# Kernel optimization log

Hardware: AMD Instinct MI355X
Metric: run time of the kernel (lower is better)

## Reference

```python
import jax, jax.numpy as jnp
import numpy as np

BS, N, M, D = 4, 8192, 8192, 3

def setup_inputs() -> dict:
    key = jax.random.key(0)
    k1, k2 = jax.random.split(key)
    preds = jax.random.normal(k1, (BS, M, D), dtype=jnp.float32)
    gts = jax.random.normal(k2, (BS, N, D), dtype=jnp.float32)
    mask = jnp.ones((BS, M), dtype=jnp.float32)
    return {"preds": preds, "gts": gts, "mask": mask}

def _pairwise_dist(x, y):
    # x: [bs, N, d] (gts), y: [bs, M, d] (preds)
    # P[b,n,m] = ||x_n||^2 + ||y_m||^2 - 2 x_n . y_m
    rx = jnp.sum(x * x, axis=-1)            # [bs, N] (diag of x @ x^T)
    ry = jnp.sum(y * y, axis=-1)            # [bs, M] (diag of y @ y^T)
    zz = jnp.einsum('bnd,bmd->bnm', x, y)   # [bs, N, M]
    return rx[:, :, None] + ry[:, None, :] - 2.0 * zz

def reference(preds, gts, mask):
    P = _pairwise_dist(gts, preds)          # [bs, N, M]; mask unused (as in source)
    return (jnp.min(P, axis=1),             # [bs, M] min over gts for each pred
            jnp.min(P, axis=2),             # [bs, N] min over preds for each gt
            jnp.argmin(P, axis=1),          # [bs, M]
            jnp.argmin(P, axis=2))          # [bs, N]
```

## Files before the change

### kernel.cpp

```cpp
#include <hip/hip_runtime.h>

#pragma clang fp contract(off)


#define BS     4
#define NPTS   8192
#define CHUNK  2048
#define BLOCK  1024
#define SPLITS 32
#define SLOTS  32
#define QT     8
#define QBLK   (SLOTS * QT)
#define ROWS   (CHUNK / SPLITS)

typedef float f32x2 __attribute__((ext_vector_type(2)));

__global__ __launch_bounds__(BLOCK, 4)
void chamfer_kernel(const float* __restrict__ preds,
                    const float* __restrict__ gts,
                    float* __restrict__ out)
{
#pragma clang fp contract(off)
    const int dir   = blockIdx.z;
    const int b     = blockIdx.y;
    const int t     = threadIdx.x;
    const int slot  = t & (SLOTS - 1);
    const int split = t >> 5;
    const int qb    = blockIdx.x * QBLK;

    const float* qbase = (dir == 0 ? preds : gts) + (size_t)b * NPTS * 3;
    const float* rbase = (dir == 0 ? gts : preds) + (size_t)b * NPTS * 3;
    float* outv = out + (size_t)dir       * BS * NPTS + (size_t)b * NPTS;
    float* outi = out + (size_t)(2 + dir) * BS * NPTS + (size_t)b * NPTS;

    __shared__ alignas(16) float smem[12288];
    float (*sh)[4]        = (float (*)[4])smem;
    float *shv            = smem;
    unsigned short *shi16 = (unsigned short *)(smem + 8192);

    f32x2 qxv[4], qyv[4], qzv[4], rqv[4];
#pragma unroll
    for (int g = 0; g < 4; ++g) {
#pragma unroll
        for (int h = 0; h < 2; ++h) {
            const int j = g * 2 + h;
            const int q = qb + j * SLOTS + slot;
            const float x = qbase[(size_t)q * 3 + 0];
            const float y = qbase[(size_t)q * 3 + 1];
            const float z = qbase[(size_t)q * 3 + 2];
            qxv[g][h] = x; qyv[g][h] = y; qzv[g][h] = z;
            const float a0 = x * x;
            const float a1 = y * y;
            const float a2 = z * z;
            rqv[g][h] = (a0 + a1) + a2;
        }
    }

    float bestv[QT];
    int   besti[QT];
#pragma unroll
    for (int j = 0; j < QT; ++j) { bestv[j] = 3.0e38f; besti[j] = 0; }

    const int nchunks = NPTS / CHUNK;
    for (int c = 0; c < nchunks; ++c) {
        __syncthreads();
#pragma unroll
        for (int u = 0; u < CHUNK / BLOCK; ++u) {
            const int i = u * BLOCK + t;
            const size_t n = (size_t)c * CHUNK + i;
            const float x = rbase[n * 3 + 0];
            const float y = rbase[n * 3 + 1];
            const float z = rbase[n * 3 + 2];
            sh[i][0] = x;
            sh[i][1] = y;
            sh[i][2] = z;
            const float a0 = x * x;
            const float a1 = y * y;
            const float a2 = z * z;
            sh[i][3] = (a0 + a1) + a2;
        }
        __syncthreads();

        const int row0 = split * ROWS;
        const int idxb = c * CHUNK + row0;
#pragma unroll 4
        for (int k = 0; k < ROWS; ++k) {
            const int row = row0 + k;
            const float x  = sh[row][0];
            const float y  = sh[row][1];
            const float z  = sh[row][2];
            const float rr = sh[row][3];
            const int idx = idxb + k;
#pragma unroll
            for (int g = 0; g < 4; ++g) {
                const f32x2 p0 = qxv[g] * x;
                const f32x2 p1 = qyv[g] * y;
                const f32x2 p2 = qzv[g] * z;
                const f32x2 zz = (p0 + p1) + p2;
                const f32x2 ts = rqv[g] + rr;
                const f32x2 w  = zz * 2.0f;
                const f32x2 v  = ts - w;
                if (v[0] < bestv[2 * g + 0]) { bestv[2 * g + 0] = v[0]; besti[2 * g + 0] = idx; }
                if (v[1] < bestv[2 * g + 1]) { bestv[2 * g + 1] = v[1]; besti[2 * g + 1] = idx; }
            }
        }
    }

    __syncthreads();
#pragma unroll
    for (int j = 0; j < QT; ++j) {
        shv  [split * QBLK + j * SLOTS + slot] = bestv[j];
        shi16[split * QBLK + j * SLOTS + slot] = (unsigned short)besti[j];
    }
    __syncthreads();

    const int qloc = t >> 2;
    const int sl   = t & 3;
    float bv = 3.0e38f;
    int   bi = 0;
#pragma unroll
    for (int k = 0; k < SPLITS / 4; ++k) {
        const int s = sl + k * 4;
        const float v2 = shv[s * QBLK + qloc];
        const int   i2 = shi16[s * QBLK + qloc];
        if (v2 < bv || (v2 == bv && i2 < bi)) { bv = v2; bi = i2; }
    }
#pragma unroll
    for (int o = 1; o < 4; o <<= 1) {
        const float ov = __shfl_xor(bv, o);
        const int   oi = __shfl_xor(bi, o);
        if (ov < bv || (ov == bv && oi < bi)) { bv = ov; bi = oi; }
    }
    if (sl == 0) {
        outv[qb + qloc] = bv;
        outi[qb + qloc] = (float)bi;
    }
}

extern "C" void kernel_launch(void* const* d_in, const int* in_sizes, int n_in,
                              void* d_out, int out_size, void* d_ws, size_t ws_size,
                              hipStream_t stream)
{
    const float* preds = (const float*)d_in[0];
    const float* gts   = (const float*)d_in[1];
    float* out = (float*)d_out;

    dim3 grid(NPTS / QBLK, BS, 2);
    dim3 block(BLOCK);
    chamfer_kernel<<<grid, block, 0, stream>>>(preds, gts, out);
}
```

Before: 116.9 us.

## Split reference set into halves with workspace partials and a finalize kernel

The nearest-neighbour search now splits the reference points into two halves. It launches four times as many smaller blocks (512 threads, 128 queries each), each writing its partial min/argmin to a workspace. A small finalize kernel then merges the two halves with a lowest-index tie-break. The goal is more blocks and waves per CU, so the latency of the compare-and-select loop is better hidden. The shared tile is also packed as float4 with padding to cut LDS bank conflicts. The cost is an extra launch and a workspace round trip, and the old single-kernel path is kept as a fallback when the workspace is too small.

```diff
diff --git a/kernel.cpp b/kernel.cpp
--- a/kernel.cpp
+++ b/kernel.cpp
@@ -5,38 +5,40 @@
 
 #define BS     4
 #define NPTS   8192
-#define CHUNK  2048
-#define BLOCK  1024
+#define BLOCK  512
+#define SLOTS  16
 #define SPLITS 32
-#define SLOTS  32
 #define QT     8
 #define QBLK   (SLOTS * QT)
+#define HALF   4096
+#define CHUNK  1024
 #define ROWS   (CHUNK / SPLITS)
 
 typedef float f32x2 __attribute__((ext_vector_type(2)));
+typedef float f32x4 __attribute__((ext_vector_type(4)));
 
 __global__ __launch_bounds__(BLOCK, 4)
-void chamfer_kernel(const float* __restrict__ preds,
-                    const float* __restrict__ gts,
-                    float* __restrict__ out)
+void chamfer_part(const float* __restrict__ preds,
+                  const float* __restrict__ gts,
+                  float* __restrict__ wsv,
+                  unsigned* __restrict__ wsi)
 {
 #pragma clang fp contract(off)
-    const int dir   = blockIdx.z;
-    const int b     = blockIdx.y;
-    const int t     = threadIdx.x;
+    const int dir  = blockIdx.z & 1;
+    const int half = blockIdx.z >> 1;
+    const int b    = blockIdx.y;
+    const int qb   = blockIdx.x * QBLK;
+    const int t    = threadIdx.x;
     const int slot  = t & (SLOTS - 1);
-    const int split = t >> 5;
-    const int qb    = blockIdx.x * QBLK;
+    const int split = t >> 4;
 
     const float* qbase = (dir == 0 ? preds : gts) + (size_t)b * NPTS * 3;
     const float* rbase = (dir == 0 ? gts : preds) + (size_t)b * NPTS * 3;
-    float* outv = out + (size_t)dir       * BS * NPTS + (size_t)b * NPTS;
-    float* outi = out + (size_t)(2 + dir) * BS * NPTS + (size_t)b * NPTS;
-
-    __shared__ alignas(16) float smem[12288];
-    float (*sh)[4]        = (float (*)[4])smem;
-    float *shv            = smem;
-    unsigned short *shi16 = (unsigned short *)(smem + 8192);
+
+    __shared__ alignas(16) float smem[6144];
+    f32x4* tile4          = (f32x4*)smem;
+    float* shv            = smem;
+    unsigned short* shi16 = (unsigned short*)(smem + 4096);
 
     f32x2 qxv[4], qyv[4], qzv[4], rqv[4];
 #pragma unroll
@@ -61,35 +63,34 @@
 #pragma unroll
     for (int j = 0; j < QT; ++j) { bestv[j] = 3.0e38f; besti[j] = 0; }
 
-    const int nchunks = NPTS / CHUNK;
-    for (int c = 0; c < nchunks; ++c) {
+    for (int c = 0; c < HALF / CHUNK; ++c) {
+        const int n0 = half * HALF + c * CHUNK;
         __syncthreads();
 #pragma unroll
         for (int u = 0; u < CHUNK / BLOCK; ++u) {
             const int i = u * BLOCK + t;
-            const size_t n = (size_t)c * CHUNK + i;
+            const size_t n = (size_t)n0 + i;
             const float x = rbase[n * 3 + 0];
             const float y = rbase[n * 3 + 1];
             const float z = rbase[n * 3 + 2];
-            sh[i][0] = x;
-            sh[i][1] = y;
-            sh[i][2] = z;
             const float a0 = x * x;
             const float a1 = y * y;
             const float a2 = z * z;
-            sh[i][3] = (a0 + a1) + a2;
-        }
-        __syncthreads();
-
-        const int row0 = split * ROWS;
-        const int idxb = c * CHUNK + row0;
+            const float rr = (a0 + a1) + a2;
+            const int sp = i + (i >> 5);
+            tile4[sp] = (f32x4){x, y, z, rr};
+        }
+        __syncthreads();
+
+        const int sbase = split * (ROWS + 1);
+        const int idxb  = n0 + split * ROWS;
 #pragma unroll 4
         for (int k = 0; k < ROWS; ++k) {
-            const int row = row0 + k;
-            const float x  = sh[row][0];
-            const float y  = sh[row][1];
-            const float z  = sh[row][2];
-            const float rr = sh[row][3];
+            const f32x4 cand = tile4[sbase + k];
+            const float x  = cand[0];
+            const float y  = cand[1];
+            const float z  = cand[2];
+            const float rr = cand[3];
             const int idx = idxb + k;
 #pragma unroll
             for (int g = 0; g < 4; ++g) {
@@ -132,9 +133,138 @@
         if (ov < bv || (ov == bv && oi < bi)) { bv = ov; bi = oi; }
     }
     if (sl == 0) {
-        outv[qb + qloc] = bv;
-        outi[qb + qloc] = (float)bi;
-    }
+        const size_t g = ((size_t)(dir * BS + b) * NPTS + qb + qloc);
+        wsv[g * 2 + half] = bv;
+        wsi[g * 2 + half] = (unsigned)bi;
+    }
+}
+
+__global__ __launch_bounds__(256)
+void chamfer_fin(const float* __restrict__ wsv,
+                 const unsigned* __restrict__ wsi,
+                 float* __restrict__ out)
+{
+    const int g = blockIdx.x * 256 + threadIdx.x;
+    const float v0 = wsv[2 * g + 0];
+    const float v1 = wsv[2 * g + 1];
+    const unsigned i0 = wsi[2 * g + 0];
+    const unsigned i1 = wsi[2 * g + 1];
+    const bool take1 = (v1 < v0) || (v1 == v0 && i1 < i0);
+    out[g]         = take1 ? v1 : v0;
+    out[65536 + g] = (float)(take1 ? i1 : i0);
+}
+
+#define FCHUNK  2048
+#define FBLOCK  1024
+#define FSPLITS 32
+#define FSLOTS  32
+#define FQBLK   (FSLOTS * QT)
+#define FROWS   (FCHUNK / FSPLITS)
+
+__global__ __launch_bounds__(FBLOCK, 4)
+void chamfer_single(const float* __restrict__ preds,
+                    const float* __restrict__ gts,
+                    float* __restrict__ out)
+{
+#pragma clang fp contract(off)
+    const int dir   = blockIdx.z;
+    const int b     = blockIdx.y;
+    const int t     = threadIdx.x;
+    const int slot  = t & (FSLOTS - 1);
+    const int split = t >> 5;
+    const int qb    = blockIdx.x * FQBLK;
+
+    const float* qbase = (dir == 0 ? preds : gts) + (size_t)b * NPTS * 3;
+    const float* rbase = (dir == 0 ? gts : preds) + (size_t)b * NPTS * 3;
+    float* outv = out + (size_t)dir       * BS * NPTS + (size_t)b * NPTS;
+    float* outi = out + (size_t)(2 + dir) * BS * NPTS + (size_t)b * NPTS;
+
+    __shared__ alignas(16) float smem[12288];
+    float (*sh)[4]        = (float (*)[4])smem;
+    float *shv            = smem;
+    unsigned short *shi16 = (unsigned short *)(smem + 8192);
+
+    f32x2 qxv[4], qyv[4], qzv[4], rqv[4];
+#pragma unroll
+    for (int g = 0; g < 4; ++g) {
+#pragma unroll
+        for (int h = 0; h < 2; ++h) {
+            const int j = g * 2 + h;
+            const int q = qb + j * FSLOTS + slot;
+            const float x = qbase[(size_t)q * 3 + 0];
+            const float y = qbase[(size_t)q * 3 + 1];
+            const float z = qbase[(size_t)q * 3 + 2];
+            qxv[g][h] = x; qyv[g][h] = y; qzv[g][h] = z;
+            const float a0 = x * x, a1 = y * y, a2 = z * z;
+            rqv[g][h] = (a0 + a1) + a2;
+        }
+    }
+
+    float bestv[QT]; int besti[QT];
+#pragma unroll
+    for (int j = 0; j < QT; ++j) { bestv[j] = 3.0e38f; besti[j] = 0; }
+
+    for (int c = 0; c < NPTS / FCHUNK; ++c) {
+        __syncthreads();
+#pragma unroll
+        for (int u = 0; u < FCHUNK / FBLOCK; ++u) {
+            const int i = u * FBLOCK + t;
+            const size_t n = (size_t)c * FCHUNK + i;
+            const float x = rbase[n * 3 + 0];
+            const float y = rbase[n * 3 + 1];
+            const float z = rbase[n * 3 + 2];
+            sh[i][0] = x; sh[i][1] = y; sh[i][2] = z;
+            const float a0 = x * x, a1 = y * y, a2 = z * z;
+            sh[i][3] = (a0 + a1) + a2;
+        }
+        __syncthreads();
+        const int row0 = split * FROWS;
+        const int idxb = c * FCHUNK + row0;
+#pragma unroll 4
+        for (int k = 0; k < FROWS; ++k) {
+            const int row = row0 + k;
+            const float x = sh[row][0], y = sh[row][1];
+            const float z = sh[row][2], rr = sh[row][3];
+            const int idx = idxb + k;
+#pragma unroll
+            for (int g = 0; g < 4; ++g) {
+                const f32x2 p0 = qxv[g] * x;
+                const f32x2 p1 = qyv[g] * y;
+                const f32x2 p2 = qzv[g] * z;
+                const f32x2 zz = (p0 + p1) + p2;
+                const f32x2 ts = rqv[g] + rr;
+                const f32x2 w  = zz * 2.0f;
+                const f32x2 v  = ts - w;
+                if (v[0] < bestv[2 * g + 0]) { bestv[2 * g + 0] = v[0]; besti[2 * g + 0] = idx; }
+                if (v[1] < bestv[2 * g + 1]) { bestv[2 * g + 1] = v[1]; besti[2 * g + 1] = idx; }
+            }
+        }
+    }
+
+    __syncthreads();
+#pragma unroll
+    for (int j = 0; j < QT; ++j) {
+        shv  [split * FQBLK + j * FSLOTS + slot] = bestv[j];
+        shi16[split * FQBLK + j * FSLOTS + slot] = (unsigned short)besti[j];
+    }
+    __syncthreads();
+    const int qloc = t >> 2;
+    const int sl   = t & 3;
+    float bv = 3.0e38f; int bi = 0;
+#pragma unroll
+    for (int k = 0; k < FSPLITS / 4; ++k) {
+        const int s = sl + k * 4;
+        const float v2 = shv[s * FQBLK + qloc];
+        const int   i2 = shi16[s * FQBLK + qloc];
+        if (v2 < bv || (v2 == bv && i2 < bi)) { bv = v2; bi = i2; }
+    }
+#pragma unroll
+    for (int o = 1; o < 4; o <<= 1) {
+        const float ov = __shfl_xor(bv, o);
+        const int   oi = __shfl_xor(bi, o);
+        if (ov < bv || (ov == bv && oi < bi)) { bv = ov; bi = oi; }
+    }
+    if (sl == 0) { outv[qb + qloc] = bv; outi[qb + qloc] = (float)bi; }
 }
 
 extern "C" void kernel_launch(void* const* d_in, const int* in_sizes, int n_in,
@@ -145,7 +275,16 @@
     const float* gts   = (const float*)d_in[1];
     float* out = (float*)d_out;
 
-    dim3 grid(NPTS / QBLK, BS, 2);
-    dim3 block(BLOCK);
-    chamfer_kernel<<<grid, block, 0, stream>>>(preds, gts, out);
-}
+    const size_t nkeys = (size_t)2 * BS * NPTS * 2;
+    const size_t need  = nkeys * (sizeof(float) + sizeof(unsigned));
+    if (ws_size >= need) {
+        float*    wsv = (float*)d_ws;
+        unsigned* wsi = (unsigned*)((float*)d_ws + nkeys);
+        chamfer_part<<<dim3(NPTS / QBLK, BS, 4), BLOCK, 0, stream>>>(
+            preds, gts, wsv, wsi);
+        chamfer_fin<<<dim3(2 * BS * NPTS / 256), 256, 0, stream>>>(wsv, wsi, out);
+    } else {
+        chamfer_single<<<dim3(NPTS / FQBLK, BS, 2), FBLOCK, 0, stream>>>(
+            preds, gts, out);
+    }
+}
```

Result: no change. 116.5 us (-0.3%).
